# Performance work log

Hardware: AMD Instinct MI355X
Metric: run time of the kernel (lower is better)

The kernel has to match this reference:

```python
import jax, jax.numpy as jnp
import numpy as np

N_NODES = 50000
N_EDGES = 1600000
IN_FEATS = 128
HIDDEN = 32
HEADS = 4
N_GRAPHS = 64
NEG_SLOPE = 0.2


def setup_inputs() -> dict:
    key = jax.random.key(0)
    ks = jax.random.split(key, 10)
    features = jax.random.normal(ks[0], (N_NODES, IN_FEATS), dtype=jnp.float32)
    src = jax.random.randint(ks[1], (N_EDGES,), 0, N_NODES, dtype=jnp.int32)
    dst = jax.random.randint(ks[2], (N_EDGES,), 0, N_NODES, dtype=jnp.int32)
    graph_ids = jnp.sort(jax.random.randint(ks[3], (N_NODES,), 0, N_GRAPHS, dtype=jnp.int32))
    # GATConv params (fc has no bias in DGL; conv bias added post-aggregation)
    s = 1.0 / np.sqrt(IN_FEATS)
    W = jax.random.uniform(ks[4], (IN_FEATS, HEADS * HIDDEN), jnp.float32, -s, s)
    attn_l = jax.random.normal(ks[5], (HEADS, HIDDEN), dtype=jnp.float32) * 0.1
    attn_r = jax.random.normal(ks[6], (HEADS, HIDDEN), dtype=jnp.float32) * 0.1
    bias = jnp.zeros((HEADS * HIDDEN,), dtype=jnp.float32)
    s2 = 1.0 / np.sqrt(HEADS * HIDDEN)
    fc_w = jax.random.uniform(ks[7], (HEADS * HIDDEN, 1), jnp.float32, -s2, s2)
    fc_b = jnp.zeros((1,), dtype=jnp.float32)
    return dict(features=features, src=src, dst=dst, graph_ids=graph_ids,
                W=W, attn_l=attn_l, attn_r=attn_r, bias=bias, fc_w=fc_w, fc_b=fc_b)


def reference(features, src, dst, graph_ids, W, attn_l, attn_r, bias, fc_w, fc_b):
    N = features.shape[0]
    H, D = attn_l.shape
    feat = (features @ W).reshape(N, H, D)              # [N,H,D]
    el = jnp.sum(feat * attn_l[None], axis=-1)          # [N,H]
    er = jnp.sum(feat * attn_r[None], axis=-1)          # [N,H]
    e = jax.nn.leaky_relu(el[src] + er[dst], NEG_SLOPE) # [E,H]
    # edge softmax over incoming edges of each dst node
    m = jax.ops.segment_max(e, dst, num_segments=N)     # [N,H]
    ex = jnp.exp(e - m[dst])
    denom = jax.ops.segment_sum(ex, dst, num_segments=N)
    a = ex / denom[dst]                                 # [E,H]
    msg = feat[src] * a[:, :, None]                     # [E,H,D]
    rst = jax.ops.segment_sum(msg, dst, num_segments=N) # [N,H,D]
    h = rst.reshape(N, H * D) + bias[None, :]
    # dropout(p=0.5) treated as identity (eval mode)
    h = jax.nn.elu(h)
    counts = jax.ops.segment_sum(jnp.ones((N,), h.dtype), graph_ids, num_segments=N_GRAPHS)
    hg = jax.ops.segment_sum(h, graph_ids, num_segments=N_GRAPHS) / counts[:, None]
    y = jax.nn.sigmoid(hg @ fc_w + fc_b[None, :])       # [G,1]
    return y
```

## Files before the change

kernel.cpp:

```cpp
#include <hip/hip_runtime.h>
#include <hip/hip_bf16.h>
#include <math.h>

#define N_NODES 50000
#define N_EDGES 1600000
#define HEADS 4
#define HIDDEN 32
#define N_GRAPHS 64
#define NEG_SLOPE 0.2f
#define NT_SCAN ((N_NODES + 255) / 256)

#define OFS_FEAT 0
#define OFS_TICK 0
#define OFS_EL   6400000
#define OFS_ER   6600000
#define OFS_P    6800000
#define OFS_CNT  6850000
#define OFS_OFF  6900000
#define OFS_TS   6950016
#define OFS_SRC  6950272

#define GLD16(g, l)                                                            \
  __builtin_amdgcn_global_load_lds(                                            \
      (const __attribute__((address_space(1))) void*)(g),                      \
      (__attribute__((address_space(3))) void*)(l), 16, 0, 0)

__device__ __forceinline__ unsigned pack_bf16x2(float a, float b) {
  __hip_bfloat16 ha = __float2bfloat16(a), hb = __float2bfloat16(b);
  unsigned ua = *(const unsigned short*)&ha, ub = *(const unsigned short*)&hb;
  return ua | (ub << 16);
}
__device__ __forceinline__ float bf16_lo(unsigned u) {
  unsigned v = u << 16; return *(const float*)&v;
}
__device__ __forceinline__ float bf16_hi(unsigned u) {
  unsigned v = u & 0xFFFF0000u; return *(const float*)&v;
}

#define FMA4(A, XS, WV)                                                        \
  A.x = fmaf(XS, WV.x, A.x);                                                   \
  A.y = fmaf(XS, WV.y, A.y);                                                   \
  A.z = fmaf(XS, WV.z, A.z);                                                   \
  A.w = fmaf(XS, WV.w, A.w);

#define DOT4(A, B) ((A).x * (B).x + (A).y * (B).y + (A).z * (B).z + (A).w * (B).w)

__global__ __launch_bounds__(256, 2) void k_gemm(
    const float* __restrict__ X, const float* __restrict__ W,
    const float* __restrict__ attn_l, const float* __restrict__ attn_r,
    unsigned* __restrict__ featb, float* __restrict__ el, float* __restrict__ er) {
  __shared__ float Wl[128 * 128];
  __shared__ float Xl[32 * 128];
  const int t = threadIdx.x;
  const int lane = t & 63;
  const int wave = t >> 6;

  for (int i = 0; i < 16; ++i) {
    int chunk = i * 4 + wave;
    GLD16(W + chunk * 256 + lane * 4, Wl + chunk * 256);
  }

  const int u = t & 31;
  const int gn = t >> 5;
  const int h = u >> 3;
  const float4 al = *(const float4*)&attn_l[h * 32 + 4 * (u & 7)];
  const float4 ar = *(const float4*)&attn_r[h * 32 + 4 * (u & 7)];
  const int ntiles = (N_NODES + 31) / 32;
  __syncthreads();

  for (int tile = blockIdx.x; tile < ntiles; tile += gridDim.x) {
    const int n0 = tile * 32;
    if (n0 + 32 <= N_NODES) {
      for (int i = 0; i < 4; ++i) {
        int chunk = i * 4 + wave;
        GLD16(X + n0 * 128 + chunk * 256 + lane * 4, Xl + chunk * 256);
      }
    } else {
      for (int i = t; i < 1024; i += 256) {
        int row = i >> 5, kq = i & 31;
        float4 v = make_float4(0.f, 0.f, 0.f, 0.f);
        if (n0 + row < N_NODES)
          v = ((const float4*)(X + (size_t)(n0 + row) * 128))[kq];
        ((float4*)Xl)[i] = v;
      }
    }
    __syncthreads();

    float4 a0 = make_float4(0.f, 0.f, 0.f, 0.f);
    float4 a1 = a0, a2 = a0, a3 = a0;
#pragma unroll 4
    for (int k = 0; k < 128; k += 4) {
      float4 w0 = *(const float4*)&Wl[(k + 0) * 128 + 4 * u];
      float4 w1 = *(const float4*)&Wl[(k + 1) * 128 + 4 * u];
      float4 w2 = *(const float4*)&Wl[(k + 2) * 128 + 4 * u];
      float4 w3 = *(const float4*)&Wl[(k + 3) * 128 + 4 * u];
      float4 x0 = *(const float4*)&Xl[(gn * 4 + 0) * 128 + k];
      float4 x1 = *(const float4*)&Xl[(gn * 4 + 1) * 128 + k];
      float4 x2 = *(const float4*)&Xl[(gn * 4 + 2) * 128 + k];
      float4 x3 = *(const float4*)&Xl[(gn * 4 + 3) * 128 + k];
      FMA4(a0, x0.x, w0) FMA4(a0, x0.y, w1) FMA4(a0, x0.z, w2) FMA4(a0, x0.w, w3)
      FMA4(a1, x1.x, w0) FMA4(a1, x1.y, w1) FMA4(a1, x1.z, w2) FMA4(a1, x1.w, w3)
      FMA4(a2, x2.x, w0) FMA4(a2, x2.y, w1) FMA4(a2, x2.z, w2) FMA4(a2, x2.w, w3)
      FMA4(a3, x3.x, w0) FMA4(a3, x3.y, w1) FMA4(a3, x3.z, w2) FMA4(a3, x3.w, w3)
    }
    const int nb = n0 + gn * 4;
    if (nb + 0 < N_NODES)
      *(uint2*)&featb[(size_t)(nb + 0) * 64 + 2 * u] =
          make_uint2(pack_bf16x2(a0.x, a0.y), pack_bf16x2(a0.z, a0.w));
    if (nb + 1 < N_NODES)
      *(uint2*)&featb[(size_t)(nb + 1) * 64 + 2 * u] =
          make_uint2(pack_bf16x2(a1.x, a1.y), pack_bf16x2(a1.z, a1.w));
    if (nb + 2 < N_NODES)
      *(uint2*)&featb[(size_t)(nb + 2) * 64 + 2 * u] =
          make_uint2(pack_bf16x2(a2.x, a2.y), pack_bf16x2(a2.z, a2.w));
    if (nb + 3 < N_NODES)
      *(uint2*)&featb[(size_t)(nb + 3) * 64 + 2 * u] =
          make_uint2(pack_bf16x2(a3.x, a3.y), pack_bf16x2(a3.z, a3.w));

    float pl0 = DOT4(a0, al), pl1 = DOT4(a1, al), pl2 = DOT4(a2, al), pl3 = DOT4(a3, al);
    float pr0 = DOT4(a0, ar), pr1 = DOT4(a1, ar), pr2 = DOT4(a2, ar), pr3 = DOT4(a3, ar);
#pragma unroll
    for (int m = 1; m < 8; m <<= 1) {
      pl0 += __shfl_xor(pl0, m, 64); pl1 += __shfl_xor(pl1, m, 64);
      pl2 += __shfl_xor(pl2, m, 64); pl3 += __shfl_xor(pl3, m, 64);
      pr0 += __shfl_xor(pr0, m, 64); pr1 += __shfl_xor(pr1, m, 64);
      pr2 += __shfl_xor(pr2, m, 64); pr3 += __shfl_xor(pr3, m, 64);
    }
    if ((u & 7) == 0) {
      if (nb + 0 < N_NODES) { el[(nb + 0) * 4 + h] = pl0; er[(nb + 0) * 4 + h] = pr0; }
      if (nb + 1 < N_NODES) { el[(nb + 1) * 4 + h] = pl1; er[(nb + 1) * 4 + h] = pr1; }
      if (nb + 2 < N_NODES) { el[(nb + 2) * 4 + h] = pl2; er[(nb + 2) * 4 + h] = pr2; }
      if (nb + 3 < N_NODES) { el[(nb + 3) * 4 + h] = pl3; er[(nb + 3) * 4 + h] = pr3; }
    }
    __syncthreads();
  }
}

__global__ void k_ticket(const int* __restrict__ dst, int* __restrict__ cnt,
                         int* __restrict__ tick) {
  int e2 = blockIdx.x * 256 + threadIdx.x;
  if (e2 * 2 >= N_EDGES) return;
  int2 d = ((const int2*)dst)[e2];
  int t0 = atomicAdd(&cnt[d.x], 1);
  int t1 = atomicAdd(&cnt[d.y], 1);
  ((int2*)tick)[e2] = make_int2(t0, t1);
}

__global__ void k_scan1(const int* __restrict__ cnt, int* __restrict__ tsum) {
  __shared__ int sh[256];
  int i = blockIdx.x * 256 + threadIdx.x;
  sh[threadIdx.x] = (i < N_NODES) ? cnt[i] : 0;
  __syncthreads();
  for (int s = 128; s > 0; s >>= 1) {
    if (threadIdx.x < s) sh[threadIdx.x] += sh[threadIdx.x + s];
    __syncthreads();
  }
  if (threadIdx.x == 0) tsum[blockIdx.x] = sh[0];
}

__global__ void k_scan2(int* tsum) {
  __shared__ int sh[256];
  int t = threadIdx.x;
  int v = (t < NT_SCAN) ? tsum[t] : 0;
  sh[t] = v;
  __syncthreads();
  for (int s = 1; s < 256; s <<= 1) {
    int add = (t >= s) ? sh[t - s] : 0;
    __syncthreads();
    sh[t] += add;
    __syncthreads();
  }
  if (t < NT_SCAN) tsum[t] = sh[t] - v;
}

__global__ void k_scan3(const int* __restrict__ cnt, const int* __restrict__ tsum,
                        int* __restrict__ off) {
  __shared__ int sh[256];
  int t = threadIdx.x;
  int i = blockIdx.x * 256 + t;
  int v = (i < N_NODES) ? cnt[i] : 0;
  sh[t] = v;
  __syncthreads();
  for (int s = 1; s < 256; s <<= 1) {
    int add = (t >= s) ? sh[t - s] : 0;
    __syncthreads();
    sh[t] += add;
    __syncthreads();
  }
  int excl = sh[t] - v + tsum[blockIdx.x];
  if (i < N_NODES) {
    off[i] = excl;
    if (i == N_NODES - 1) off[N_NODES] = excl + v;
  }
}

__global__ void k_place(const int* __restrict__ src, const int* __restrict__ dst,
                        const int* __restrict__ off, const int* __restrict__ tick,
                        int* __restrict__ srcbuf) {
  int e2 = blockIdx.x * 256 + threadIdx.x;
  if (e2 * 2 >= N_EDGES) return;
  int2 s = ((const int2*)src)[e2];
  int2 d = ((const int2*)dst)[e2];
  int2 t = ((const int2*)tick)[e2];
  int o0 = off[d.x];
  int o1 = off[d.y];
  srcbuf[o0 + t.x] = s.x;
  srcbuf[o1 + t.y] = s.y;
}

__global__ __launch_bounds__(256) void k_aggregate(
    const unsigned* __restrict__ featb, const float* __restrict__ el,
    const float* __restrict__ er, const int* __restrict__ off,
    const int* __restrict__ srcbuf, const float* __restrict__ bias,
    const float* __restrict__ fc_w, float* __restrict__ pbuf) {
  int gid = blockIdx.x * blockDim.x + threadIdx.x;
  int v = gid >> 6;
  if (v >= N_NODES) return;
  const int lane = threadIdx.x & 63;
  const int sub = lane & 15;
  const int par = lane >> 4;
  const int h = sub >> 2;

  const float erv = er[v * 4 + h];
  const int start = off[v], end = off[v + 1];

  float sum = 0.f;
  float acc0 = 0.f, acc1 = 0.f, acc2 = 0.f, acc3 = 0.f;
  float acc4 = 0.f, acc5 = 0.f, acc6 = 0.f, acc7 = 0.f;

  int iA = start + par;
  if (iA < end) {
    int sA = srcbuf[iA];
    float eA = el[sA * 4 + h];
    uint4 fA = *(const uint4*)&featb[(size_t)sA * 64 + sub * 4];

    int iB = iA + 4;
    bool hasB = iB < end;
    float eB = 0.f; uint4 fB = make_uint4(0, 0, 0, 0);
    if (hasB) {
      int sB = srcbuf[iB];
      eB = el[sB * 4 + h];
      fB = *(const uint4*)&featb[(size_t)sB * 64 + sub * 4];
    }

    while (true) {
      const int iC = iB + 4;
      const bool hasC = iC < end;
      float eC = 0.f; uint4 fC = make_uint4(0, 0, 0, 0);
      if (hasC) {
        int sC = srcbuf[iC];
        eC = el[sC * 4 + h];
        fC = *(const uint4*)&featb[(size_t)sC * 64 + sub * 4];
      }

      float e = eA + erv;
      e = (e > 0.f) ? e : NEG_SLOPE * e;
      float p = __expf(e);
      sum += p;
      acc0 = fmaf(bf16_lo(fA.x), p, acc0);
      acc1 = fmaf(bf16_hi(fA.x), p, acc1);
      acc2 = fmaf(bf16_lo(fA.y), p, acc2);
      acc3 = fmaf(bf16_hi(fA.y), p, acc3);
      acc4 = fmaf(bf16_lo(fA.z), p, acc4);
      acc5 = fmaf(bf16_hi(fA.z), p, acc5);
      acc6 = fmaf(bf16_lo(fA.w), p, acc6);
      acc7 = fmaf(bf16_hi(fA.w), p, acc7);

      if (!hasB) break;
      eA = eB; fA = fB;
      iB = iC; hasB = hasC; eB = eC; fB = fC;
    }
  }

#pragma unroll
  for (int mk = 16; mk < 64; mk <<= 1) {
    sum += __shfl_xor(sum, mk, 64);
    acc0 += __shfl_xor(acc0, mk, 64);
    acc1 += __shfl_xor(acc1, mk, 64);
    acc2 += __shfl_xor(acc2, mk, 64);
    acc3 += __shfl_xor(acc3, mk, 64);
    acc4 += __shfl_xor(acc4, mk, 64);
    acc5 += __shfl_xor(acc5, mk, 64);
    acc6 += __shfl_xor(acc6, mk, 64);
    acc7 += __shfl_xor(acc7, mk, 64);
  }

  const float inv = (end > start) ? 1.f / sum : 0.f;
  const float4 b4a = *(const float4*)&bias[sub * 8];
  const float4 b4b = *(const float4*)&bias[sub * 8 + 4];
  const float4 w4a = *(const float4*)&fc_w[sub * 8];
  const float4 w4b = *(const float4*)&fc_w[sub * 8 + 4];
  float r0 = fmaf(acc0, inv, b4a.x);
  float r1 = fmaf(acc1, inv, b4a.y);
  float r2 = fmaf(acc2, inv, b4a.z);
  float r3 = fmaf(acc3, inv, b4a.w);
  float r4 = fmaf(acc4, inv, b4b.x);
  float r5 = fmaf(acc5, inv, b4b.y);
  float r6 = fmaf(acc6, inv, b4b.z);
  float r7 = fmaf(acc7, inv, b4b.w);
  r0 = (r0 > 0.f) ? r0 : __expf(r0) - 1.f;
  r1 = (r1 > 0.f) ? r1 : __expf(r1) - 1.f;
  r2 = (r2 > 0.f) ? r2 : __expf(r2) - 1.f;
  r3 = (r3 > 0.f) ? r3 : __expf(r3) - 1.f;
  r4 = (r4 > 0.f) ? r4 : __expf(r4) - 1.f;
  r5 = (r5 > 0.f) ? r5 : __expf(r5) - 1.f;
  r6 = (r6 > 0.f) ? r6 : __expf(r6) - 1.f;
  r7 = (r7 > 0.f) ? r7 : __expf(r7) - 1.f;
  float t = r0 * w4a.x + r1 * w4a.y + r2 * w4a.z + r3 * w4a.w +
            r4 * w4b.x + r5 * w4b.y + r6 * w4b.z + r7 * w4b.w;
#pragma unroll
  for (int mk = 1; mk < 16; mk <<= 1) t += __shfl_xor(t, mk, 64);
  if (lane == 0) pbuf[v] = t;
}

__global__ void k_pool(const float* __restrict__ pbuf, const int* __restrict__ gids,
                       const float* __restrict__ fc_b, float* __restrict__ y) {
  int g = blockIdx.x;
  int a = 0, b = N_NODES;
  while (a < b) { int mid = (a + b) >> 1; if (gids[mid] < g) a = mid + 1; else b = mid; }
  int lo = a;
  b = N_NODES;
  while (a < b) { int mid = (a + b) >> 1; if (gids[mid] < g + 1) a = mid + 1; else b = mid; }
  int hi = a;

  float s = 0.f;
  for (int i = lo + threadIdx.x; i < hi; i += blockDim.x) s += pbuf[i];
  __shared__ float sh[256];
  sh[threadIdx.x] = s;
  __syncthreads();
  for (int st = 128; st > 0; st >>= 1) {
    if (threadIdx.x < st) sh[threadIdx.x] += sh[threadIdx.x + st];
    __syncthreads();
  }
  if (threadIdx.x == 0) {
    float cnt = (float)(hi - lo);
    float hg = sh[0] / cnt;
    float x = hg + fc_b[0];
    y[g] = 1.f / (1.f + expf(-x));
  }
}

extern "C" void kernel_launch(void* const* d_in, const int* in_sizes, int n_in,
                              void* d_out, int out_size, void* d_ws, size_t ws_size,
                              hipStream_t stream) {
  const float* features = (const float*)d_in[0];
  const int* src = (const int*)d_in[1];
  const int* dst = (const int*)d_in[2];
  const int* gids = (const int*)d_in[3];
  const float* W = (const float*)d_in[4];
  const float* attn_l = (const float*)d_in[5];
  const float* attn_r = (const float*)d_in[6];
  const float* bias = (const float*)d_in[7];
  const float* fc_w = (const float*)d_in[8];
  const float* fc_b = (const float*)d_in[9];

  float* ws = (float*)d_ws;
  unsigned* featb = (unsigned*)d_ws + OFS_FEAT;
  float* el = ws + OFS_EL;
  float* er = ws + OFS_ER;
  float* pbuf = ws + OFS_P;
  int* tick = (int*)d_ws + OFS_TICK;
  int* cnt = (int*)d_ws + OFS_CNT;
  int* off = (int*)d_ws + OFS_OFF;
  int* tsum = (int*)d_ws + OFS_TS;
  int* srcbuf = (int*)d_ws + OFS_SRC;

  hipMemsetAsync(cnt, 0, N_NODES * sizeof(int), stream);

  k_ticket<<<(N_EDGES / 2 + 255) / 256, 256, 0, stream>>>(dst, cnt, tick);
  k_scan1<<<NT_SCAN, 256, 0, stream>>>(cnt, tsum);
  k_scan2<<<1, 256, 0, stream>>>(tsum);
  k_scan3<<<NT_SCAN, 256, 0, stream>>>(cnt, tsum, off);
  k_place<<<(N_EDGES / 2 + 255) / 256, 256, 0, stream>>>(src, dst, off, tick, srcbuf);

  k_gemm<<<512, 256, 0, stream>>>(features, W, attn_l, attn_r, featb, el, er);

  k_aggregate<<<(N_NODES * 64) / 256 + 1, 256, 0, stream>>>(featb, el, er, off, srcbuf,
                                                            bias, fc_w, pbuf);
  k_pool<<<N_GRAPHS, 256, 0, stream>>>(pbuf, gids, fc_b, (float*)d_out);
}
```

Baseline: 292.6 us.

## Replace atomic-ticket CSR build with two-level bucket sort by destination

Builds the dst-sorted CSR with a two-pass bucket sort instead of per-edge global atomics. Edges are first split into 196 coarse buckets of 256 nodes each using LDS histograms and one global atomic per bucket per block. A per-bucket 1024-thread block then sorts its edges locally into srcbuf and writes the offsets. This removes 1.6M contended global atomics and the scattered off[] lookups, at the cost of an extra int2 staging pass through ebuf and a nondeterministic edge order within each node.

Result: faster. 253.7 us (-13.3%).

```diff
diff --git a/kernel.cpp b/kernel.cpp
--- a/kernel.cpp
+++ b/kernel.cpp
@@ -8,16 +8,21 @@
 #define HIDDEN 32
 #define N_GRAPHS 64
 #define NEG_SLOPE 0.2f
-#define NT_SCAN ((N_NODES + 255) / 256)
+
+#define NBUCK 196
+#define BKT_EPT 8
+#define BKT_CHUNK (256 * BKT_EPT)
+#define NBKB ((N_EDGES + BKT_CHUNK - 1) / BKT_CHUNK)
 
 #define OFS_FEAT 0
-#define OFS_TICK 0
+#define OFS_EBUF 0
 #define OFS_EL   6400000
 #define OFS_ER   6600000
 #define OFS_P    6800000
-#define OFS_CNT  6850000
+#define OFS_GCNT 6850000
+#define OFS_GBASE 6850256
+#define OFS_GPOS 6850512
 #define OFS_OFF  6900000
-#define OFS_TS   6950016
 #define OFS_SRC  6950272
 
 #define GLD16(g, l)                                                            \
@@ -136,32 +141,26 @@
   }
 }
 
-__global__ void k_ticket(const int* __restrict__ dst, int* __restrict__ cnt,
-                         int* __restrict__ tick) {
-  int e2 = blockIdx.x * 256 + threadIdx.x;
-  if (e2 * 2 >= N_EDGES) return;
-  int2 d = ((const int2*)dst)[e2];
-  int t0 = atomicAdd(&cnt[d.x], 1);
-  int t1 = atomicAdd(&cnt[d.y], 1);
-  ((int2*)tick)[e2] = make_int2(t0, t1);
-}
-
-__global__ void k_scan1(const int* __restrict__ cnt, int* __restrict__ tsum) {
+__global__ void k_bhist(const int* __restrict__ dst, int* __restrict__ gcount) {
+  __shared__ int lh[NBUCK];
+  const int t = threadIdx.x;
+  if (t < NBUCK) lh[t] = 0;
+  __syncthreads();
+  const int base = blockIdx.x * BKT_CHUNK;
+#pragma unroll
+  for (int j = 0; j < BKT_EPT; ++j) {
+    int e = base + j * 256 + t;
+    if (e < N_EDGES) atomicAdd(&lh[dst[e] >> 8], 1);
+  }
+  __syncthreads();
+  if (t < NBUCK && lh[t] > 0) atomicAdd(&gcount[t], lh[t]);
+}
+
+__global__ void k_bscan(const int* __restrict__ gcount, int* __restrict__ gbase,
+                        int* __restrict__ gpos) {
   __shared__ int sh[256];
-  int i = blockIdx.x * 256 + threadIdx.x;
-  sh[threadIdx.x] = (i < N_NODES) ? cnt[i] : 0;
-  __syncthreads();
-  for (int s = 128; s > 0; s >>= 1) {
-    if (threadIdx.x < s) sh[threadIdx.x] += sh[threadIdx.x + s];
-    __syncthreads();
-  }
-  if (threadIdx.x == 0) tsum[blockIdx.x] = sh[0];
-}
-
-__global__ void k_scan2(int* tsum) {
-  __shared__ int sh[256];
-  int t = threadIdx.x;
-  int v = (t < NT_SCAN) ? tsum[t] : 0;
+  const int t = threadIdx.x;
+  int v = (t < NBUCK) ? gcount[t] : 0;
   sh[t] = v;
   __syncthreads();
   for (int s = 1; s < 256; s <<= 1) {
@@ -170,42 +169,77 @@
     sh[t] += add;
     __syncthreads();
   }
-  if (t < NT_SCAN) tsum[t] = sh[t] - v;
-}
-
-__global__ void k_scan3(const int* __restrict__ cnt, const int* __restrict__ tsum,
-                        int* __restrict__ off) {
-  __shared__ int sh[256];
-  int t = threadIdx.x;
-  int i = blockIdx.x * 256 + t;
-  int v = (i < N_NODES) ? cnt[i] : 0;
-  sh[t] = v;
+  int excl = sh[t] - v;
+  if (t < NBUCK) { gbase[t] = excl; gpos[t] = excl; }
+  if (t == NBUCK - 1) gbase[NBUCK] = excl + v;
+}
+
+__global__ void k_bucket(const int* __restrict__ src, const int* __restrict__ dst,
+                         int* __restrict__ gpos, int2* __restrict__ ebuf) {
+  __shared__ int lh[NBUCK];
+  __shared__ int lbase[NBUCK];
+  const int t = threadIdx.x;
+  if (t < NBUCK) lh[t] = 0;
+  __syncthreads();
+  const int base = blockIdx.x * BKT_CHUNK;
+  int s8[BKT_EPT], d8[BKT_EPT], r8[BKT_EPT], b8[BKT_EPT];
+#pragma unroll
+  for (int j = 0; j < BKT_EPT; ++j) {
+    int e = base + j * 256 + t;
+    bool ok = e < N_EDGES;
+    s8[j] = ok ? src[e] : 0;
+    d8[j] = ok ? dst[e] : 0;
+    b8[j] = d8[j] >> 8;
+    int r = 0;
+    if (ok) r = atomicAdd(&lh[b8[j]], 1);
+    r8[j] = r;
+  }
+  __syncthreads();
+  if (t < NBUCK && lh[t] > 0) lbase[t] = atomicAdd(&gpos[t], lh[t]);
+  __syncthreads();
+#pragma unroll
+  for (int j = 0; j < BKT_EPT; ++j) {
+    int e = base + j * 256 + t;
+    if (e < N_EDGES) ebuf[lbase[b8[j]] + r8[j]] = make_int2(s8[j], d8[j]);
+  }
+}
+
+__global__ __launch_bounds__(1024) void k_bsort(
+    const int2* __restrict__ ebuf, const int* __restrict__ gbase,
+    int* __restrict__ srcbuf, int* __restrict__ off) {
+  __shared__ int lcnt[256];
+  __shared__ int loff[256];
+  __shared__ int lpos[256];
+  const int t = threadIdx.x;
+  const int b = blockIdx.x;
+  const int lo = gbase[b], hi = gbase[b + 1];
+  if (t < 256) lcnt[t] = 0;
+  __syncthreads();
+  for (int i = lo + t; i < hi; i += 1024)
+    atomicAdd(&lcnt[ebuf[i].y & 255], 1);
+  __syncthreads();
+  int v = (t < 256) ? lcnt[t] : 0;
+  if (t < 256) loff[t] = v;
   __syncthreads();
   for (int s = 1; s < 256; s <<= 1) {
-    int add = (t >= s) ? sh[t - s] : 0;
-    __syncthreads();
-    sh[t] += add;
-    __syncthreads();
-  }
-  int excl = sh[t] - v + tsum[blockIdx.x];
-  if (i < N_NODES) {
-    off[i] = excl;
-    if (i == N_NODES - 1) off[N_NODES] = excl + v;
-  }
-}
-
-__global__ void k_place(const int* __restrict__ src, const int* __restrict__ dst,
-                        const int* __restrict__ off, const int* __restrict__ tick,
-                        int* __restrict__ srcbuf) {
-  int e2 = blockIdx.x * 256 + threadIdx.x;
-  if (e2 * 2 >= N_EDGES) return;
-  int2 s = ((const int2*)src)[e2];
-  int2 d = ((const int2*)dst)[e2];
-  int2 t = ((const int2*)tick)[e2];
-  int o0 = off[d.x];
-  int o1 = off[d.y];
-  srcbuf[o0 + t.x] = s.x;
-  srcbuf[o1 + t.y] = s.y;
+    int add = (t >= s && t < 256) ? loff[t - s] : 0;
+    __syncthreads();
+    if (t < 256) loff[t] += add;
+    __syncthreads();
+  }
+  if (t < 256) {
+    int excl = loff[t] - v;
+    lpos[t] = excl;
+    int node = b * 256 + t;
+    if (node < N_NODES) off[node] = lo + excl;
+  }
+  if (b == NBUCK - 1 && t == 0) off[N_NODES] = N_EDGES;
+  __syncthreads();
+  for (int i = lo + t; i < hi; i += 1024) {
+    int2 e = ebuf[i];
+    int p = atomicAdd(&lpos[e.y & 255], 1);
+    srcbuf[lo + p] = e.x;
+  }
 }
 
 __global__ __launch_bounds__(256) void k_aggregate(
@@ -356,22 +390,22 @@
 
   float* ws = (float*)d_ws;
   unsigned* featb = (unsigned*)d_ws + OFS_FEAT;
+  int2* ebuf = (int2*)((int*)d_ws + OFS_EBUF);
   float* el = ws + OFS_EL;
   float* er = ws + OFS_ER;
   float* pbuf = ws + OFS_P;
-  int* tick = (int*)d_ws + OFS_TICK;
-  int* cnt = (int*)d_ws + OFS_CNT;
+  int* gcount = (int*)d_ws + OFS_GCNT;
+  int* gbase = (int*)d_ws + OFS_GBASE;
+  int* gpos = (int*)d_ws + OFS_GPOS;
   int* off = (int*)d_ws + OFS_OFF;
-  int* tsum = (int*)d_ws + OFS_TS;
   int* srcbuf = (int*)d_ws + OFS_SRC;
 
-  hipMemsetAsync(cnt, 0, N_NODES * sizeof(int), stream);
-
-  k_ticket<<<(N_EDGES / 2 + 255) / 256, 256, 0, stream>>>(dst, cnt, tick);
-  k_scan1<<<NT_SCAN, 256, 0, stream>>>(cnt, tsum);
-  k_scan2<<<1, 256, 0, stream>>>(tsum);
-  k_scan3<<<NT_SCAN, 256, 0, stream>>>(cnt, tsum, off);
-  k_place<<<(N_EDGES / 2 + 255) / 256, 256, 0, stream>>>(src, dst, off, tick, srcbuf);
+  hipMemsetAsync(gcount, 0, NBUCK * sizeof(int), stream);
+
+  k_bhist<<<NBKB, 256, 0, stream>>>(dst, gcount);
+  k_bscan<<<1, 256, 0, stream>>>(gcount, gbase, gpos);
+  k_bucket<<<NBKB, 256, 0, stream>>>(src, dst, gpos, ebuf);
+  k_bsort<<<NBUCK, 1024, 0, stream>>>(ebuf, gbase, srcbuf, off);
 
   k_gemm<<<512, 256, 0, stream>>>(features, W, attn_l, attn_r, featb, el, er);
 
```
